# Performance work log

Hardware: AMD Instinct MI355X
Metric: run time of the kernel (lower is better)

Reference implementation:

```python
import jax, jax.numpy as jnp
import numpy as np

FEAT_DIM = 256
DEPTH = 2
N = 8192


def setup_inputs() -> dict:
    key = jax.random.key(0)
    ks = jax.random.split(key, 5)
    bd = 1.0 / FEAT_DIM
    X = jax.random.normal(ks[0], (N, FEAT_DIM), dtype=jnp.float32)
    coefs = jax.random.normal(ks[1], (N,), dtype=jnp.float32)
    linear = jax.random.uniform(ks[2], (DEPTH, FEAT_DIM), minval=-bd, maxval=bd, dtype=jnp.float32)
    dirv = jax.random.uniform(ks[3], (DEPTH, FEAT_DIM), minval=-bd, maxval=bd, dtype=jnp.float32)
    feat = jax.random.uniform(ks[4], (DEPTH, FEAT_DIM), minval=-bd, maxval=bd, dtype=jnp.float32)
    return {"X": X, "coefs": coefs, "linear": linear, "dirv": dirv, "feat": feat}


def reference(X, coefs, linear, dirv, feat):
    # coefs is unused: the torch forward returns before the coef_embed branch.
    emb = X
    n = X.shape[0]
    for i in range(linear.shape[0]):  # depth: small fixed loop
        # torch: emb3[j,a,k] = linear[a]*emb[j,k]; q = sum_a feat[a]*emb3 = (feat.linear)*emb
        a = jnp.dot(feat[i], linear[i])
        b = jnp.dot(dirv[i], linear[i])
        q = a * emb                      # [N, F]
        k = b * emb                      # [N, F]
        k_norm = k / jnp.linalg.norm(k)  # global Frobenius norm, as torch.norm(k)
        inner = jnp.sum(q * k_norm, axis=-1)            # [N]
        scale = jnp.where(inner <= 0, inner, 0.0)       # inner * (inner<=0)
        emb = q - scale[:, None] * k_norm
        # graph_block: X_up[i] = X[i] + (X@X[i]) @ (X - X[i]) / N
        # == X + (S@X - rowsum(S)*X)/N with S = X X^T
        S = emb @ emb.T                                 # [N, N]
        emb = emb + (S @ emb - jnp.sum(S, axis=1, keepdims=True) * emb) / n
    out = jnp.mean(emb @ emb.T, axis=-1)[:-1]           # [N-1]
    return out
```

## Files before the change

### kernel.cpp

```cpp
#include <hip/hip_runtime.h>
#include <math.h>

constexpr int NROW = 8192;
constexpr int FD   = 256;
constexpr int NZ   = 16;

typedef unsigned short u16;
typedef __attribute__((ext_vector_type(8))) short short8;
typedef __attribute__((ext_vector_type(4))) float f32x4;


__device__ __forceinline__ float f_of(float nj, float A, float B, float AB) {
    float inner = AB * nj;
    return A - (inner <= 0.f ? inner : 0.f) * B;
}
__device__ __forceinline__ float wred(float s) {
    #pragma unroll
    for (int off = 32; off; off >>= 1) s += __shfl_xor(s, off);
    return s;
}
__device__ __forceinline__ float dot4(float4 a, float4 b) {
    return a.x*b.x + a.y*b.y + a.z*b.z + a.w*b.w;
}
__device__ __forceinline__ u16 f2bf(float x) {
    unsigned int u = __float_as_uint(x);
    u = (u + 0x7FFFu + ((u >> 16) & 1u)) >> 16;
    return (u16)u;
}

__global__ void k_norm(const float* __restrict__ in, float* __restrict__ nrm,
                       float* __restrict__ fpart) {
    __shared__ float bs[4];
    int wave = threadIdx.x >> 6, lane = threadIdx.x & 63;
    int row = blockIdx.x * 4 + wave;
    const float4 v = *(const float4*)&in[(size_t)row * FD + lane * 4];
    float s = wred(dot4(v, v));
    if (lane == 0) { nrm[row] = s; bs[wave] = s; }
    __syncthreads();
    if (threadIdx.x == 0) fpart[blockIdx.x] = bs[0] + bs[1] + bs[2] + bs[3];
}

__global__ void __launch_bounds__(256, 2)
k_prep(const float* __restrict__ X, const float* __restrict__ nrm0,
       const float* __restrict__ fpart, const float* __restrict__ linear,
       const float* __restrict__ dirv, const float* __restrict__ feat,
       float* __restrict__ scal, float* __restrict__ f0,
       u16* __restrict__ Rbf, u16* __restrict__ Rt, float* __restrict__ cpart) {
    __shared__ u16 T[64][264];
    __shared__ float cred[4][256];
    __shared__ float l[256];
    __shared__ float ff[64];
    __shared__ float sdot[4];
    const int tid = threadIdx.x;
    const int r0 = blockIdx.x * 64;
    if (tid < 64) {
        for (int i = 0; i < 2; ++i) {
            float pa = 0.f, pb = 0.f;
            for (int k = tid; k < FD; k += 64) {
                float ll = linear[i*FD + k];
                pa += feat[i*FD + k] * ll;
                pb += dirv[i*FD + k] * ll;
            }
            pa = wred(pa); pb = wred(pb);
            if (tid == 0) { sdot[i] = pa; sdot[2 + i] = pb; }
        }
    }
    float s = 0.f;
    #pragma unroll
    for (int k = 0; k < 8; ++k) s += fpart[tid + k * 256];
    l[tid] = s;
    __syncthreads();
    for (int off = 128; off; off >>= 1) {
        if (tid < off) l[tid] += l[tid + off];
        __syncthreads();
    }
    const float F2 = l[0];
    const float a = sdot[0], b = sdot[2];
    const float sb = (b > 0.f) ? 1.f : ((b < 0.f) ? -1.f : 0.f);
    const float B = sb / sqrtf(F2);
    const float A = a, AB = a * B;
    if (blockIdx.x == 0 && tid == 0) {
        scal[0] = sdot[0]; scal[1] = sdot[1]; scal[2] = sdot[2]; scal[3] = sdot[3];
        scal[4] = A; scal[5] = B; scal[6] = AB; scal[7] = F2;
    }
    if (tid < 64) {
        float f = f_of(nrm0[r0 + tid], A, B, AB);
        ff[tid] = f;
        f0[r0 + tid] = f;
    }
    __syncthreads();
    const int cg = (tid & 63) * 4;
    const int rg = tid >> 6;
    float4 csum = make_float4(0.f, 0.f, 0.f, 0.f);
    for (int i = 0; i < 16; ++i) {
        int row = rg * 16 + i;
        float4 v = *(const float4*)&X[(size_t)(r0 + row) * FD + cg];
        float f = ff[row];
        v.x *= f; v.y *= f; v.z *= f; v.w *= f;
        csum.x += v.x; csum.y += v.y; csum.z += v.z; csum.w += v.w;
        unsigned lo = (unsigned)f2bf(v.x) | ((unsigned)f2bf(v.y) << 16);
        unsigned hi = (unsigned)f2bf(v.z) | ((unsigned)f2bf(v.w) << 16);
        uint2 pk = make_uint2(lo, hi);
        *(uint2*)&Rbf[(size_t)(r0 + row) * FD + cg] = pk;
        *(uint2*)&T[row][cg] = pk;
    }
    *(float4*)&cred[rg][cg] = csum;
    __syncthreads();
    cpart[(size_t)blockIdx.x * FD + tid] =
        cred[0][tid] + cred[1][tid] + cred[2][tid] + cred[3][tid];
    const int c = tid;
    #pragma unroll
    for (int ch = 0; ch < 8; ++ch) {
        unsigned w0 = (unsigned)T[ch*8+0][c] | ((unsigned)T[ch*8+1][c] << 16);
        unsigned w1 = (unsigned)T[ch*8+2][c] | ((unsigned)T[ch*8+3][c] << 16);
        unsigned w2 = (unsigned)T[ch*8+4][c] | ((unsigned)T[ch*8+5][c] << 16);
        unsigned w3 = (unsigned)T[ch*8+6][c] | ((unsigned)T[ch*8+7][c] << 16);
        uint4 o = make_uint4(w0, w1, w2, w3);
        *(uint4*)&Rt[(size_t)c * NROW + r0 + ch * 8] = o;
    }
}

__global__ void __launch_bounds__(256, 2)
k_gram(const u16* __restrict__ Rt, float* __restrict__ Gp) {
    const int bi = blockIdx.x, bj = blockIdx.y, z = blockIdx.z;
    const int tid = threadIdx.x, w = tid >> 6, lane = tid & 63;
    const int l15 = lane & 15, quad = lane >> 4;
    const int m0 = bi * 64 + (w & 1) * 32;
    const int n0 = bj * 64 + (w >> 1) * 32;
    const size_t kbase = (size_t)z * 512 + quad * 8;
    const u16* am0 = Rt + (size_t)(m0 + l15) * NROW + kbase;
    const u16* am1 = am0 + (size_t)16 * NROW;
    const u16* bn0 = Rt + (size_t)(n0 + l15) * NROW + kbase;
    const u16* bn1 = bn0 + (size_t)16 * NROW;
    f32x4 acc[2][2] = {};
    #pragma unroll
    for (int s = 0; s < 16; ++s) {
        int ko = s * 32;
        short8 a0 = *(const short8*)(am0 + ko);
        short8 a1 = *(const short8*)(am1 + ko);
        short8 b0 = *(const short8*)(bn0 + ko);
        short8 b1 = *(const short8*)(bn1 + ko);
        acc[0][0] = __builtin_amdgcn_mfma_f32_16x16x32_bf16(a0, b0, acc[0][0], 0, 0, 0);
        acc[0][1] = __builtin_amdgcn_mfma_f32_16x16x32_bf16(a0, b1, acc[0][1], 0, 0, 0);
        acc[1][0] = __builtin_amdgcn_mfma_f32_16x16x32_bf16(a1, b0, acc[1][0], 0, 0, 0);
        acc[1][1] = __builtin_amdgcn_mfma_f32_16x16x32_bf16(a1, b1, acc[1][1], 0, 0, 0);
    }
    float* gz = Gp + (size_t)z * (FD * FD);
    #pragma unroll
    for (int mi = 0; mi < 2; ++mi)
        #pragma unroll
        for (int ni = 0; ni < 2; ++ni)
            #pragma unroll
            for (int r = 0; r < 4; ++r)
                gz[(size_t)(m0 + mi*16 + quad*4 + r) * FD + n0 + ni*16 + l15] =
                    acc[mi][ni][r];
}

__global__ void k_gred(const float* __restrict__ Gp, u16* __restrict__ Gbf) {
    size_t e0 = (size_t)blockIdx.x * 256 + threadIdx.x;
    float s = 0.f;
    #pragma unroll
    for (int z = 0; z < NZ; ++z) s += Gp[(size_t)z * (FD * FD) + e0];
    Gbf[e0] = f2bf(s);
}

__global__ void __launch_bounds__(256, 2)
k_apply(const float* __restrict__ X, const u16* __restrict__ Rbf,
        const u16* __restrict__ Gbf, const float* __restrict__ f0,
        const float* __restrict__ cpart, float* __restrict__ emb,
        float* __restrict__ nrm1, float* __restrict__ fpart1,
        float* __restrict__ cpart1, float* __restrict__ wpart1) {
    __shared__ float Sl[32][260];
    __shared__ float csh[FD];
    __shared__ float u0s[32], ffs[32], nrs[32];
    __shared__ float nw8[32][8];
    const int tid = threadIdx.x, w = tid >> 6, lane = tid & 63;
    const int l15 = lane & 15, quad = lane >> 4;
    const int r0 = blockIdx.x * 32;

    {
        float s = 0.f;
        #pragma unroll 8
        for (int b = 0; b < 128; ++b) s += cpart[(size_t)b * FD + tid];
        csh[tid] = s;
    }
    if (tid < 32) ffs[tid] = f0[r0 + tid];
    __syncthreads();
    #pragma unroll
    for (int jj = 0; jj < 8; ++jj) {
        int row = w * 8 + jj;
        float4 xv = *(const float4*)&X[(size_t)(r0 + row) * FD + lane * 4];
        float4 cv = *(const float4*)&csh[lane * 4];
        float t = wred(dot4(xv, cv));
        if (lane == 0) u0s[row] = ffs[row] * t;
    }
    const u16* ap0 = Rbf + (size_t)(r0 + l15) * FD + quad * 8;
    const u16* ap1 = ap0 + (size_t)16 * FD;
    const int n0w = w * 64;
    const u16* bp = Gbf + (size_t)(n0w + l15) * FD + quad * 8;
    f32x4 acc[2][4] = {};
    #pragma unroll
    for (int s = 0; s < 8; ++s) {
        int ko = s * 32;
        short8 a0 = *(const short8*)(ap0 + ko);
        short8 a1 = *(const short8*)(ap1 + ko);
        short8 b0 = *(const short8*)(bp + ko);
        short8 b1 = *(const short8*)(bp + 16 * FD + ko);
        short8 b2 = *(const short8*)(bp + 32 * FD + ko);
        short8 b3 = *(const short8*)(bp + 48 * FD + ko);
        acc[0][0] = __builtin_amdgcn_mfma_f32_16x16x32_bf16(a0, b0, acc[0][0], 0, 0, 0);
        acc[0][1] = __builtin_amdgcn_mfma_f32_16x16x32_bf16(a0, b1, acc[0][1], 0, 0, 0);
        acc[0][2] = __builtin_amdgcn_mfma_f32_16x16x32_bf16(a0, b2, acc[0][2], 0, 0, 0);
        acc[0][3] = __builtin_amdgcn_mfma_f32_16x16x32_bf16(a0, b3, acc[0][3], 0, 0, 0);
        acc[1][0] = __builtin_amdgcn_mfma_f32_16x16x32_bf16(a1, b0, acc[1][0], 0, 0, 0);
        acc[1][1] = __builtin_amdgcn_mfma_f32_16x16x32_bf16(a1, b1, acc[1][1], 0, 0, 0);
        acc[1][2] = __builtin_amdgcn_mfma_f32_16x16x32_bf16(a1, b2, acc[1][2], 0, 0, 0);
        acc[1][3] = __builtin_amdgcn_mfma_f32_16x16x32_bf16(a1, b3, acc[1][3], 0, 0, 0);
    }
    #pragma unroll
    for (int mi = 0; mi < 2; ++mi)
        #pragma unroll
        for (int ni = 0; ni < 4; ++ni)
            #pragma unroll
            for (int r = 0; r < 4; ++r)
                Sl[mi*16 + quad*4 + r][n0w + ni*16 + l15] = acc[mi][ni][r];
    __syncthreads();
    const float invN = 1.0f / NROW;
    float er[32];
    float csum = 0.f;
    #pragma unroll
    for (int j = 0; j < 32; ++j) {
        float x = X[(size_t)(r0 + j) * FD + tid];
        float rv = ffs[j] * x;
        float e = rv + (Sl[j][tid] - u0s[j] * rv) * invN;
        emb[(size_t)(r0 + j) * FD + tid] = e;
        er[j] = e;
        csum += e;
        Sl[j][tid] = e * e;
    }
    __syncthreads();
    {
        int row = tid & 31, q = tid >> 5;
        float pn = 0.f;
        #pragma unroll
        for (int i = 0; i < 32; ++i) pn += Sl[row][q * 32 + i];
        nw8[row][q] = pn;
    }
    __syncthreads();
    if (tid < 32) {
        float nn = 0.f;
        #pragma unroll
        for (int q = 0; q < 8; ++q) nn += nw8[tid][q];
        nrm1[r0 + tid] = nn;
        nrs[tid] = nn;
    }
    __syncthreads();
    float wsum = 0.f;
    #pragma unroll
    for (int j = 0; j < 32; ++j) wsum += nrs[j] * er[j];
    cpart1[(size_t)blockIdx.x * FD + tid] = csum;
    wpart1[(size_t)blockIdx.x * FD + tid] = wsum;
    if (tid == 0) {
        float fp = 0.f;
        #pragma unroll
        for (int j = 0; j < 32; ++j) fp += nrs[j];
        fpart1[blockIdx.x] = fp;
    }
}

__device__ __forceinline__ void red1_scal(const float* fpart1, const float* scal,
                                          float* l, float& A, float& B, float& AB,
                                          float& kap) {
    int tid = threadIdx.x;
    l[tid] = fpart1[tid];
    __syncthreads();
    for (int off = 128; off; off >>= 1) {
        if (tid < off) l[tid] += l[tid + off];
        __syncthreads();
    }
    float F2 = l[0];
    float a = scal[1], b = scal[3];
    float sb = (b > 0.f) ? 1.f : ((b < 0.f) ? -1.f : 0.f);
    B = sb / sqrtf(F2);
    A = a; AB = a * B;
    kap = (AB <= 0.f) ? AB * B : 0.f;
    __syncthreads();
}

__global__ void k_sv(const float* __restrict__ fpart1, const float* __restrict__ scal,
                     const float* __restrict__ cpart1, const float* __restrict__ wpart1,
                     float* __restrict__ svec) {
    __shared__ float l[256];
    float A1, B1, AB1, kap;
    red1_scal(fpart1, scal, l, A1, B1, AB1, kap);
    int tid = threadIdx.x;
    int col = blockIdx.x * 4 + (tid >> 6);
    int lane = tid & 63;
    float cs = 0.f, wsm = 0.f;
    #pragma unroll
    for (int b = lane; b < 256; b += 64) {
        cs  += cpart1[(size_t)b * FD + col];
        wsm += wpart1[(size_t)b * FD + col];
    }
    #pragma unroll
    for (int off = 32; off; off >>= 1) {
        cs  += __shfl_down(cs, off);
        wsm += __shfl_down(wsm, off);
    }
    if (lane == 0) svec[col] = A1 * cs - kap * wsm;
}

__global__ void k_uv(const float* __restrict__ emb, const float* __restrict__ nrm1,
                     const float* __restrict__ scal, const float* __restrict__ fpart1,
                     const float* __restrict__ svec, float* __restrict__ u,
                     float* __restrict__ vpart) {
    __shared__ float l[256];
    __shared__ float ssh[FD];
    __shared__ float uf[16];
    float A, B, AB, kap;
    red1_scal(fpart1, scal, l, A, B, AB, kap);
    int tid = threadIdx.x;
    int r0 = blockIdx.x * 16;
    ssh[tid] = svec[tid];
    __syncthreads();
    const int wave = tid >> 6, lane = tid & 63;
    float4 sv = *(const float4*)&ssh[lane*4];
    #pragma unroll
    for (int jj = 0; jj < 4; ++jj) {
        int row = r0 + wave * 4 + jj;
        float4 ev = *(const float4*)&emb[(size_t)row * FD + lane*4];
        float s = wred(dot4(ev, sv));
        if (lane == 0) {
            float f = A - kap * nrm1[row];
            float uj = f * s;
            u[row] = uj;
            uf[wave*4 + jj] = uj * f;
        }
    }
    __syncthreads();
    float vp = 0.f;
    #pragma unroll
    for (int j = 0; j < 16; ++j)
        vp += uf[j] * emb[(size_t)(r0 + j) * FD + tid];
    vpart[(size_t)blockIdx.x * FD + tid] = vp;
}

__global__ void k_vred(const float* __restrict__ part, float* __restrict__ vec) {
    int tid = threadIdx.x;
    int col = blockIdx.x * 4 + (tid >> 6);
    int lane = tid & 63;
    float s = 0.f;
    #pragma unroll
    for (int b = 0; b < 8; ++b) s += part[(size_t)(b * 64 + lane) * FD + col];
    #pragma unroll
    for (int off = 32; off; off >>= 1) s += __shfl_down(s, off);
    if (lane == 0) vec[col] = s;
}

__global__ void k_out(const float* __restrict__ emb, const float* __restrict__ nrm1,
                      const float* __restrict__ scal, const float* __restrict__ fpart1,
                      const float* __restrict__ vvec, const float* __restrict__ u,
                      float* __restrict__ out) {
    __shared__ float l[256];
    __shared__ float vsh[FD];
    float A, B, AB, kap;
    red1_scal(fpart1, scal, l, A, B, AB, kap);
    int tid = threadIdx.x;
    int r0 = blockIdx.x * 16;
    vsh[tid] = vvec[tid];
    __syncthreads();
    const int wave = tid >> 6, lane = tid & 63;
    const float invN = 1.0f / NROW;
    float4 vv = *(const float4*)&vsh[lane*4];
    #pragma unroll
    for (int jj = 0; jj < 4; ++jj) {
        int row = r0 + wave * 4 + jj;
        float4 ev = *(const float4*)&emb[(size_t)row * FD + lane*4];
        float s = wred(dot4(ev, vv));
        if (lane == 0 && row < NROW - 1) {
            float f = A - kap * nrm1[row];
            float uj = u[row];
            out[row] = (uj + (f * s - uj * uj) * invN) * invN;
        }
    }
}

extern "C" void kernel_launch(void* const* d_in, const int* in_sizes, int n_in,
                              void* d_out, int out_size, void* d_ws, size_t ws_size,
                              hipStream_t stream) {
    const float* X      = (const float*)d_in[0];
    const float* linear = (const float*)d_in[2];
    const float* dirv   = (const float*)d_in[3];
    const float* feat   = (const float*)d_in[4];
    float* out = (float*)d_out;

    char* ws = (char*)d_ws;
    float* scal   = (float*)(ws + 0);
    float* nrm0   = (float*)(ws + 4096);
    float* nrm1   = (float*)(ws + 36864);
    float* fpart  = (float*)(ws + 69632);
    float* fpart1 = (float*)(ws + 77824);
    float* svec   = (float*)(ws + 78848);
    float* vvec   = (float*)(ws + 79872);
    float* u      = (float*)(ws + 81920);
    float* f0     = (float*)(ws + 114688);
    float* cpart  = (float*)(ws + 147456);
    u16*   Gbf    = (u16*)  (ws + 278528);
    float* cpart1 = (float*)(ws + 409600);
    float* wpart1 = (float*)(ws + 671744);
    float* vpart  = (float*)(ws + 933888);
    u16*   Rbf    = (u16*)  (ws + 2097152);
    u16*   Rt     = (u16*)  (ws + 6291456);
    float* Gp     = (float*)(ws + 10485760);
    float* emb    = (float*)(ws + 18874368);

    k_norm<<<NROW/4, 256, 0, stream>>>(X, nrm0, fpart);
    k_prep<<<128, 256, 0, stream>>>(X, nrm0, fpart, linear, dirv, feat,
                                    scal, f0, Rbf, Rt, cpart);
    k_gram<<<dim3(4,4,NZ), 256, 0, stream>>>(Rt, Gp);
    k_gred<<<256, 256, 0, stream>>>(Gp, Gbf);
    k_apply<<<256, 256, 0, stream>>>(X, Rbf, Gbf, f0, cpart, emb, nrm1,
                                     fpart1, cpart1, wpart1);
    k_sv<<<64, 256, 0, stream>>>(fpart1, scal, cpart1, wpart1, svec);
    k_uv<<<NROW/16, 256, 0, stream>>>(emb, nrm1, scal, fpart1, svec, u, vpart);
    k_vred<<<64, 256, 0, stream>>>(vpart, vvec);
    k_out<<<NROW/16, 256, 0, stream>>>(emb, nrm1, scal, fpart1, vvec, u, out);
}
```

Baseline: 126.5 us.

## Fuse Gram reduction into gram kernel and fold small reduction kernels

The separate Gram-partial reduction kernel is replaced by a last-block-done pattern. Each gram tile increments an atomic counter, and the final z-slice block sums the partials and writes the bf16 Gram. The svec and vvec reduction kernels are removed: k_uv and k_out now reduce the 256 partial rows per column themselves, and each block handles 32 rows instead of 16. This cuts three kernel launches and their inter-kernel gaps, at the cost of redundant per-block partial reductions and atomic/fence overhead.

```diff
diff --git a/kernel.cpp b/kernel.cpp
--- a/kernel.cpp
+++ b/kernel.cpp
@@ -44,7 +44,7 @@
 k_prep(const float* __restrict__ X, const float* __restrict__ nrm0,
        const float* __restrict__ fpart, const float* __restrict__ linear,
        const float* __restrict__ dirv, const float* __restrict__ feat,
-       float* __restrict__ scal, float* __restrict__ f0,
+       float* __restrict__ scal, int* __restrict__ cnt, float* __restrict__ f0,
        u16* __restrict__ Rbf, u16* __restrict__ Rt, float* __restrict__ cpart) {
     __shared__ u16 T[64][264];
     __shared__ float cred[4][256];
@@ -53,6 +53,7 @@
     __shared__ float sdot[4];
     const int tid = threadIdx.x;
     const int r0 = blockIdx.x * 64;
+    if (blockIdx.x == 0 && tid < 16) cnt[tid] = 0;
     if (tid < 64) {
         for (int i = 0; i < 2; ++i) {
             float pa = 0.f, pb = 0.f;
@@ -121,7 +122,9 @@
 }
 
 __global__ void __launch_bounds__(256, 2)
-k_gram(const u16* __restrict__ Rt, float* __restrict__ Gp) {
+k_gram(const u16* __restrict__ Rt, float* __restrict__ Gp,
+       u16* __restrict__ Gbf, int* __restrict__ cnt) {
+    __shared__ int oldc;
     const int bi = blockIdx.x, bj = blockIdx.y, z = blockIdx.z;
     const int tid = threadIdx.x, w = tid >> 6, lane = tid & 63;
     const int l15 = lane & 15, quad = lane >> 4;
@@ -154,14 +157,21 @@
             for (int r = 0; r < 4; ++r)
                 gz[(size_t)(m0 + mi*16 + quad*4 + r) * FD + n0 + ni*16 + l15] =
                     acc[mi][ni][r];
-}
-
-__global__ void k_gred(const float* __restrict__ Gp, u16* __restrict__ Gbf) {
-    size_t e0 = (size_t)blockIdx.x * 256 + threadIdx.x;
-    float s = 0.f;
-    #pragma unroll
-    for (int z = 0; z < NZ; ++z) s += Gp[(size_t)z * (FD * FD) + e0];
-    Gbf[e0] = f2bf(s);
+    __threadfence();
+    __syncthreads();
+    if (tid == 0) oldc = atomicAdd(&cnt[bi * 4 + bj], 1);
+    __syncthreads();
+    if (oldc == 15) {
+        __threadfence();
+        for (int idx = tid; idx < 4096; idx += 256) {
+            int m = bi * 64 + (idx >> 6), n = bj * 64 + (idx & 63);
+            float s = 0.f;
+            #pragma unroll
+            for (int zz = 0; zz < NZ; ++zz)
+                s += Gp[(size_t)zz * (FD * FD) + (size_t)m * FD + n];
+            Gbf[(size_t)m * FD + n] = f2bf(s);
+        }
+    }
 }
 
 __global__ void __launch_bounds__(256, 2)
@@ -287,96 +297,76 @@
     __syncthreads();
 }
 
-__global__ void k_sv(const float* __restrict__ fpart1, const float* __restrict__ scal,
-                     const float* __restrict__ cpart1, const float* __restrict__ wpart1,
-                     float* __restrict__ svec) {
-    __shared__ float l[256];
-    float A1, B1, AB1, kap;
-    red1_scal(fpart1, scal, l, A1, B1, AB1, kap);
-    int tid = threadIdx.x;
-    int col = blockIdx.x * 4 + (tid >> 6);
-    int lane = tid & 63;
-    float cs = 0.f, wsm = 0.f;
-    #pragma unroll
-    for (int b = lane; b < 256; b += 64) {
-        cs  += cpart1[(size_t)b * FD + col];
-        wsm += wpart1[(size_t)b * FD + col];
-    }
-    #pragma unroll
-    for (int off = 32; off; off >>= 1) {
-        cs  += __shfl_down(cs, off);
-        wsm += __shfl_down(wsm, off);
-    }
-    if (lane == 0) svec[col] = A1 * cs - kap * wsm;
-}
-
-__global__ void k_uv(const float* __restrict__ emb, const float* __restrict__ nrm1,
-                     const float* __restrict__ scal, const float* __restrict__ fpart1,
-                     const float* __restrict__ svec, float* __restrict__ u,
-                     float* __restrict__ vpart) {
+__global__ void __launch_bounds__(256, 2)
+k_uv(const float* __restrict__ emb, const float* __restrict__ nrm1,
+     const float* __restrict__ scal, const float* __restrict__ fpart1,
+     const float* __restrict__ cpart1, const float* __restrict__ wpart1,
+     float* __restrict__ u, float* __restrict__ vpart) {
     __shared__ float l[256];
     __shared__ float ssh[FD];
-    __shared__ float uf[16];
+    __shared__ float uf[32];
     float A, B, AB, kap;
     red1_scal(fpart1, scal, l, A, B, AB, kap);
-    int tid = threadIdx.x;
-    int r0 = blockIdx.x * 16;
-    ssh[tid] = svec[tid];
-    __syncthreads();
-    const int wave = tid >> 6, lane = tid & 63;
-    float4 sv = *(const float4*)&ssh[lane*4];
-    #pragma unroll
-    for (int jj = 0; jj < 4; ++jj) {
-        int row = r0 + wave * 4 + jj;
-        float4 ev = *(const float4*)&emb[(size_t)row * FD + lane*4];
+    const int tid = threadIdx.x;
+    const int r0 = blockIdx.x * 32;
+    {
+        float cs = 0.f, wsm = 0.f;
+        #pragma unroll 8
+        for (int b = 0; b < 256; ++b) {
+            cs  += cpart1[(size_t)b * FD + tid];
+            wsm += wpart1[(size_t)b * FD + tid];
+        }
+        ssh[tid] = A * cs - kap * wsm;
+    }
+    __syncthreads();
+    const int w = tid >> 6, lane = tid & 63;
+    float4 sv = *(const float4*)&ssh[lane * 4];
+    #pragma unroll
+    for (int jj = 0; jj < 8; ++jj) {
+        int j = w * 8 + jj, row = r0 + j;
+        float4 ev = *(const float4*)&emb[(size_t)row * FD + lane * 4];
         float s = wred(dot4(ev, sv));
         if (lane == 0) {
             float f = A - kap * nrm1[row];
             float uj = f * s;
             u[row] = uj;
-            uf[wave*4 + jj] = uj * f;
+            uf[j] = uj * f;
         }
     }
     __syncthreads();
     float vp = 0.f;
     #pragma unroll
-    for (int j = 0; j < 16; ++j)
+    for (int j = 0; j < 32; ++j)
         vp += uf[j] * emb[(size_t)(r0 + j) * FD + tid];
     vpart[(size_t)blockIdx.x * FD + tid] = vp;
 }
 
-__global__ void k_vred(const float* __restrict__ part, float* __restrict__ vec) {
-    int tid = threadIdx.x;
-    int col = blockIdx.x * 4 + (tid >> 6);
-    int lane = tid & 63;
-    float s = 0.f;
-    #pragma unroll
-    for (int b = 0; b < 8; ++b) s += part[(size_t)(b * 64 + lane) * FD + col];
-    #pragma unroll
-    for (int off = 32; off; off >>= 1) s += __shfl_down(s, off);
-    if (lane == 0) vec[col] = s;
-}
-
-__global__ void k_out(const float* __restrict__ emb, const float* __restrict__ nrm1,
-                      const float* __restrict__ scal, const float* __restrict__ fpart1,
-                      const float* __restrict__ vvec, const float* __restrict__ u,
-                      float* __restrict__ out) {
+__global__ void __launch_bounds__(256, 2)
+k_out(const float* __restrict__ emb, const float* __restrict__ nrm1,
+      const float* __restrict__ scal, const float* __restrict__ fpart1,
+      const float* __restrict__ vpart, const float* __restrict__ u,
+      float* __restrict__ out) {
     __shared__ float l[256];
     __shared__ float vsh[FD];
     float A, B, AB, kap;
     red1_scal(fpart1, scal, l, A, B, AB, kap);
-    int tid = threadIdx.x;
-    int r0 = blockIdx.x * 16;
-    vsh[tid] = vvec[tid];
-    __syncthreads();
-    const int wave = tid >> 6, lane = tid & 63;
+    const int tid = threadIdx.x;
+    const int r0 = blockIdx.x * 32;
+    {
+        float vv = 0.f;
+        #pragma unroll 8
+        for (int b = 0; b < 256; ++b) vv += vpart[(size_t)b * FD + tid];
+        vsh[tid] = vv;
+    }
+    __syncthreads();
+    const int w = tid >> 6, lane = tid & 63;
     const float invN = 1.0f / NROW;
-    float4 vv = *(const float4*)&vsh[lane*4];
-    #pragma unroll
-    for (int jj = 0; jj < 4; ++jj) {
-        int row = r0 + wave * 4 + jj;
-        float4 ev = *(const float4*)&emb[(size_t)row * FD + lane*4];
-        float s = wred(dot4(ev, vv));
+    float4 vv4 = *(const float4*)&vsh[lane * 4];
+    #pragma unroll
+    for (int jj = 0; jj < 8; ++jj) {
+        int row = r0 + w * 8 + jj;
+        float4 ev = *(const float4*)&emb[(size_t)row * FD + lane * 4];
+        float s = wred(dot4(ev, vv4));
         if (lane == 0 && row < NROW - 1) {
             float f = A - kap * nrm1[row];
             float uj = u[row];
@@ -396,12 +386,11 @@
 
     char* ws = (char*)d_ws;
     float* scal   = (float*)(ws + 0);
+    int*   cnt    = (int*)  (ws + 1024);
     float* nrm0   = (float*)(ws + 4096);
     float* nrm1   = (float*)(ws + 36864);
     float* fpart  = (float*)(ws + 69632);
     float* fpart1 = (float*)(ws + 77824);
-    float* svec   = (float*)(ws + 78848);
-    float* vvec   = (float*)(ws + 79872);
     float* u      = (float*)(ws + 81920);
     float* f0     = (float*)(ws + 114688);
     float* cpart  = (float*)(ws + 147456);
@@ -416,13 +405,11 @@
 
     k_norm<<<NROW/4, 256, 0, stream>>>(X, nrm0, fpart);
     k_prep<<<128, 256, 0, stream>>>(X, nrm0, fpart, linear, dirv, feat,
-                                    scal, f0, Rbf, Rt, cpart);
-    k_gram<<<dim3(4,4,NZ), 256, 0, stream>>>(Rt, Gp);
-    k_gred<<<256, 256, 0, stream>>>(Gp, Gbf);
+                                    scal, cnt, f0, Rbf, Rt, cpart);
+    k_gram<<<dim3(4,4,NZ), 256, 0, stream>>>(Rt, Gp, Gbf, cnt);
     k_apply<<<256, 256, 0, stream>>>(X, Rbf, Gbf, f0, cpart, emb, nrm1,
                                      fpart1, cpart1, wpart1);
-    k_sv<<<64, 256, 0, stream>>>(fpart1, scal, cpart1, wpart1, svec);
-    k_uv<<<NROW/16, 256, 0, stream>>>(emb, nrm1, scal, fpart1, svec, u, vpart);
-    k_vred<<<64, 256, 0, stream>>>(vpart, vvec);
-    k_out<<<NROW/16, 256, 0, stream>>>(emb, nrm1, scal, fpart1, vvec, u, out);
-}
+    k_uv<<<256, 256, 0, stream>>>(emb, nrm1, scal, fpart1, cpart1, wpart1,
+                                  u, vpart);
+    k_out<<<256, 256, 0, stream>>>(emb, nrm1, scal, fpart1, vpart, u, out);
+}
```

Measured after the change: 174.9 us. 38.2% more time.
